# Kernel optimization log

Hardware: AMD Instinct MI355X
Metric: run time of the kernel (lower is better)

## Reference

```python
import jax, jax.numpy as jnp
import numpy as np

EPS = 1e-5

def _ln(x, g, b):
    m = jnp.mean(x, axis=-1, keepdims=True)
    v = jnp.var(x, axis=-1, keepdims=True)
    return (x - m) / jnp.sqrt(v + EPS) * g + b

def setup_inputs() -> dict:
    key = jax.random.key(0)
    ks = jax.random.split(key, 16)
    B, T, N, K, d, E = 2, 12, 512, 8, 64, 64
    D = K * d
    s = 0.02
    inp = {
        "x": jax.random.normal(ks[0], (B, T, N, D), jnp.float32),
        "lapmatrix": jax.random.normal(ks[1], (N, N), jnp.float32),
        "node_embeddings": jax.random.normal(ks[2], (N, E), jnp.float32),
        "Wq": jax.random.normal(ks[3], (D, D), jnp.float32) * s,
        "bq": jnp.zeros((D,), jnp.float32),
        "Wk": jax.random.normal(ks[4], (D, D), jnp.float32) * s,
        "bk": jnp.zeros((D,), jnp.float32),
        "Wv": jax.random.normal(ks[5], (D, D), jnp.float32) * s,
        "bv": jnp.zeros((D,), jnp.float32),
        "Wo": jax.random.normal(ks[6], (D, D), jnp.float32) * s,
        "bo": jnp.zeros((D,), jnp.float32),
        "W1": jax.random.normal(ks[7], (4 * D, D), jnp.float32) * s,
        "b1": jnp.zeros((4 * D,), jnp.float32),
        "W2": jax.random.normal(ks[8], (D, 4 * D), jnp.float32) * s,
        "b2": jnp.zeros((D,), jnp.float32),
        "g1": jnp.ones((D,), jnp.float32),
        "be1": jnp.zeros((D,), jnp.float32),
        "g2": jnp.ones((D,), jnp.float32),
        "be2": jnp.zeros((D,), jnp.float32),
        "alpha": jnp.float32(1.0),
        "beta": jnp.float32(1.0),
        "k": 3,
    }
    return inp

def reference(x, lapmatrix, node_embeddings, Wq, bq, Wk, bk, Wv, bv, Wo, bo,
              W1, b1, W2, b2, g1, be1, g2, be2, alpha, beta, k):
    B, T, N, D = x.shape
    K, d = 8, D // 8
    x_raw = x
    xn = _ln(x, g1, be1)
    q = (xn @ Wq.T + bq).reshape(B, T, N, K, d)
    kk = (xn @ Wk.T + bk).reshape(B, T, N, K, d)
    v = (xn @ Wv.T + bv).reshape(B, T, N, K, d)
    # raw attention logits: [B,T,K,N,N]
    raw = jnp.einsum('btnkd,btmkd->btknm', q, kk) / jnp.sqrt(jnp.float32(d))
    # graph biases, all [N,N], broadcast over B,T,K
    supports = jax.nn.softmax(jax.nn.relu(node_embeddings @ node_embeddings.T), axis=1)
    adj = (lapmatrix != 0).astype(x.dtype)
    mask = jnp.where(adj == 0, jnp.float32(-1e9), jnp.float32(0.0))
    logits = raw + alpha * supports + beta * lapmatrix + mask
    attn = jax.nn.softmax(logits, axis=-1)  # dropout = identity in eval
    out = jnp.einsum('btknm,btmkd->btnkd', attn, v).reshape(B, T, N, D)
    x1 = x_raw + (out @ Wo.T + bo)
    h = _ln(x1, g2, be2)
    ffn = jax.nn.relu(h @ W1.T + b1) @ W2.T + b2
    return x1 + ffn
```

## Files before the change

### kernel.cpp

```cpp
#include <hip/hip_runtime.h>

typedef unsigned short u16;
typedef unsigned int   u32;
typedef __attribute__((ext_vector_type(8))) short bf16x8;
typedef __attribute__((ext_vector_type(4))) float f32x4;

#define DEV static __device__ __forceinline__

DEV float b2f(u16 u){ return __uint_as_float(((u32)u)<<16); }
DEV u16 f2b(float f){
  u32 u = __float_as_uint(f);
  u32 r = (u + 0x7FFFu + ((u>>16)&1u)) >> 16;
  return (u16)r;
}

union V8 { uint4 v; u16 s[8]; };

DEV bool is_f32(const void* dt){ return *(const u32*)dt == 0x3F800000u; }

DEV uint4 ld8_ext_bf(const void* p, size_t i, bool f32){
  if(f32){
    const float* q = (const float*)p + i;
    float4 a = *(const float4*)q, b = *(const float4*)(q+4);
    V8 r;
    r.s[0]=f2b(a.x); r.s[1]=f2b(a.y); r.s[2]=f2b(a.z); r.s[3]=f2b(a.w);
    r.s[4]=f2b(b.x); r.s[5]=f2b(b.y); r.s[6]=f2b(b.z); r.s[7]=f2b(b.w);
    return r.v;
  }
  return *(const uint4*)((const u16*)p + i);
}
DEV void ld8_ext_f(const void* p, size_t i, bool f32, float* o){
  if(f32){
    const float* q = (const float*)p + i;
    float4 a = *(const float4*)q, b = *(const float4*)(q+4);
    o[0]=a.x;o[1]=a.y;o[2]=a.z;o[3]=a.w;o[4]=b.x;o[5]=b.y;o[6]=b.z;o[7]=b.w;
  }else{
    V8 u; u.v = *(const uint4*)((const u16*)p + i);
    #pragma unroll
    for(int k=0;k<8;k++) o[k]=b2f(u.s[k]);
  }
}
DEV float ld1_ext(const void* p, size_t i, bool f32){
  return f32 ? ((const float*)p)[i] : b2f(((const u16*)p)[i]);
}
DEV float load_scalar(const void* p, bool f32){
  return f32 ? *(const float*)p : b2f(*(const u16*)p);
}

DEV void gl_lds16(const u16* g, u16* l){
  __builtin_amdgcn_global_load_lds((const __attribute__((address_space(1))) void*)g,
                                   (__attribute__((address_space(3))) void*)l, 16, 0, 0);
}

__global__ __launch_bounds__(256) void sentinel_kernel(u16* out, long n, const void* dt){
  long ne = is_f32(dt) ? 2*n : n;
  long i = (long)blockIdx.x*256 + threadIdx.x;
  if(i < ne) out[i] = 0x4442;
}

__global__ __launch_bounds__(256) void convert_w_kernel(
    const void* Wq, const void* Wk, const void* Wv, const void* Wo,
    const void* W1, const void* W2, u16* __restrict__ wbf, const void* dt)
{
  const bool f32 = is_f32(dt);
  size_t i = ((size_t)blockIdx.x*256 + threadIdx.x)*8;
  const void* src; size_t base;
  if(i < 262144){ src=Wq; base=0; }
  else if(i < 524288){ src=Wk; base=262144; }
  else if(i < 786432){ src=Wv; base=524288; }
  else if(i < 1048576){ src=Wo; base=786432; }
  else if(i < 2097152){ src=W1; base=1048576; }
  else { src=W2; base=2097152; }
  *(uint4*)(wbf + i) = ld8_ext_bf(src, i-base, f32);
}

__global__ __launch_bounds__(256) void convert_b_kernel(
    const void* bq, const void* bk, const void* bv, const void* bo,
    const void* b1, const void* b2, float* __restrict__ bfp, const void* dt)
{
  const bool f32 = is_f32(dt);
  int j = blockIdx.x*256 + threadIdx.x;
  if(j >= 4608) return;
  const void* src; int off;
  if(j < 512){ src=bq; off=0; }
  else if(j < 1024){ src=bk; off=512; }
  else if(j < 1536){ src=bv; off=1024; }
  else if(j < 2048){ src=bo; off=1536; }
  else if(j < 4096){ src=b1; off=2048; }
  else { src=b2; off=4096; }
  bfp[j] = ld1_ext(src, j-off, f32);
}

__global__ __launch_bounds__(256) void bias_kernel(
    const void* __restrict__ E, const void* __restrict__ lap,
    const void* __restrict__ alpha_p, const void* __restrict__ beta_p,
    float* __restrict__ bm, const void* dt)
{
  __shared__ u16 Et[64*520];
  __shared__ float red[8];
  const bool f32 = is_f32(dt);
  const int t = threadIdx.x, n = blockIdx.x;
  for(int i=0;i<16;i++){
    int c = t + i*256;
    int m = c >> 3, j0 = (c & 7) * 8;
    V8 u; u.v = ld8_ext_bf(E, (size_t)m*64 + j0, f32);
    #pragma unroll
    for(int jj=0;jj<8;jj++) Et[(j0+jj)*520 + m] = u.s[jj];
  }
  __syncthreads();
  const float alpha = load_scalar(alpha_p, f32);
  const float beta  = load_scalar(beta_p, f32);
  float sc0=0.f, sc1=0.f;
  const int m0 = t, m1 = t+256;
  for(int kk=0;kk<64;kk++){
    float en = b2f(Et[kk*520+n]);
    sc0 += en * b2f(Et[kk*520+m0]);
    sc1 += en * b2f(Et[kk*520+m1]);
  }
  sc0 = fmaxf(sc0, 0.f); sc1 = fmaxf(sc1, 0.f);
  float mx = fmaxf(sc0, sc1);
  for(int o=1;o<64;o<<=1) mx = fmaxf(mx, __shfl_xor(mx,o,64));
  const int wave = t>>6;
  if((t&63)==0) red[wave]=mx;
  __syncthreads();
  mx = fmaxf(fmaxf(red[0],red[1]), fmaxf(red[2],red[3]));
  float e0 = __expf(sc0-mx), e1 = __expf(sc1-mx);
  float sm = e0+e1;
  for(int o=1;o<64;o<<=1) sm += __shfl_xor(sm,o,64);
  if((t&63)==0) red[4+wave]=sm;
  __syncthreads();
  sm = red[4]+red[5]+red[6]+red[7];
  const float inv = 1.f/sm;
  float lv0 = ld1_ext(lap, (size_t)n*512+m0, f32);
  bm[n*512+m0] = alpha*e0*inv + beta*lv0 + (lv0==0.f ? -1e9f : 0.f);
  float lv1 = ld1_ext(lap, (size_t)n*512+m1, f32);
  bm[n*512+m1] = alpha*e1*inv + beta*lv1 + (lv1==0.f ? -1e9f : 0.f);
}

template<int EXTIN>
__global__ __launch_bounds__(64) void ln_kernel(const void* __restrict__ xin,
    const void* __restrict__ g, const void* __restrict__ b, u16* __restrict__ out,
    const void* dt)
{
  const bool f32 = is_f32(dt);
  const int row = blockIdx.x, lane = threadIdx.x;
  float v[8];
  if(EXTIN){
    ld8_ext_f(xin, (size_t)row*512 + lane*8, f32, v);
  }else{
    V8 u; u.v = *(const uint4*)((const u16*)xin + (size_t)row*512 + lane*8);
    #pragma unroll
    for(int i=0;i<8;i++) v[i]=b2f(u.s[i]);
  }
  float s=0.f, ss=0.f;
  #pragma unroll
  for(int i=0;i<8;i++){ s+=v[i]; ss+=v[i]*v[i]; }
  #pragma unroll
  for(int o=1;o<64;o<<=1){ s+=__shfl_xor(s,o,64); ss+=__shfl_xor(ss,o,64); }
  const float mean = s*(1.0f/512.0f);
  const float var  = ss*(1.0f/512.0f) - mean*mean;
  const float rstd = rsqrtf(var + 1e-5f);
  float gv[8], bv[8];
  ld8_ext_f(g, (size_t)lane*8, f32, gv);
  ld8_ext_f(b, (size_t)lane*8, f32, bv);
  V8 o8;
  #pragma unroll
  for(int i=0;i<8;i++) o8.s[i]=f2b((v[i]-mean)*rstd*gv[i]+bv[i]);
  *(uint4*)(out+(size_t)row*512+lane*8)=o8.v;
}

template<int RELU, int RES, int RESEXT, int OUTEXT>
__global__ __launch_bounds__(256) void gemm_nt(
    const u16* __restrict__ A, const u16* __restrict__ B,
    const float* __restrict__ bias, const void* __restrict__ resid,
    void* __restrict__ Cout, int N, int K, const void* dt)
{
  __shared__ u16 As[128*64];
  __shared__ u16 Bs[128*64];
  const bool f32 = is_f32(dt);
  const int t = threadIdx.x;
  const int wave = t>>6, lane = t&63;
  const int n0 = blockIdx.y*128, m0 = blockIdx.x*128;
  const int wr = wave>>1, wc = wave&1;

  f32x4 acc[4][4];
  #pragma unroll
  for(int i=0;i<4;i++)
    #pragma unroll
    for(int j=0;j<4;j++){ acc[i][j][0]=0.f; acc[i][j][1]=0.f; acc[i][j][2]=0.f; acc[i][j][3]=0.f; }

  const int lrow8 = lane>>3, lg = lane&7;
  const int gsw = (lg ^ lrow8)*8;
  const u16* Ag = A + (size_t)(m0+lrow8)*K + gsw;
  const u16* Bg = B + (size_t)(n0+lrow8)*K + gsw;
  const int fr = lane&15, qd = lane>>4, frk = (fr&7);

  for(int k0=0; k0<K; k0+=64){
    __syncthreads();
    #pragma unroll
    for(int i=0;i<4;i++){
      int c = wave*4+i;
      gl_lds16(Ag + (size_t)(c*8)*K + k0, &As[c*512]);
      gl_lds16(Bg + (size_t)(c*8)*K + k0, &Bs[c*512]);
    }
    __syncthreads();
    #pragma unroll
    for(int s=0;s<2;s++){
      const int slot = ((s*4+qd) ^ frk)*8;
      bf16x8 af[4], bfr[4];
      #pragma unroll
      for(int i=0;i<4;i++) af[i] = *(const bf16x8*)&As[(wr*64+i*16+fr)*64 + slot];
      #pragma unroll
      for(int j=0;j<4;j++) bfr[j] = *(const bf16x8*)&Bs[(wc*64+j*16+fr)*64 + slot];
      #pragma unroll
      for(int i=0;i<4;i++)
        #pragma unroll
        for(int j=0;j<4;j++)
          acc[i][j] = __builtin_amdgcn_mfma_f32_16x16x32_bf16(af[i], bfr[j], acc[i][j], 0,0,0);
    }
  }

  const int col16 = lane&15, rbase = (lane>>4)*4;
  #pragma unroll
  for(int i=0;i<4;i++){
    #pragma unroll
    for(int j=0;j<4;j++){
      const int gc = n0 + wc*64 + j*16 + col16;
      const float bv = bias[gc];
      #pragma unroll
      for(int r=0;r<4;r++){
        const int gr = m0 + wr*64 + i*16 + rbase + r;
        float val = acc[i][j][r] + bv;
        if(RELU) val = fmaxf(val, 0.f);
        if(RES){
          if(RESEXT) val += ld1_ext(resid, (size_t)gr*N+gc, f32);
          else       val += b2f(((const u16*)resid)[(size_t)gr*N+gc]);
        }
        if(OUTEXT && f32) ((float*)Cout)[(size_t)gr*N+gc] = val;
        else              ((u16*)Cout)[(size_t)gr*N+gc] = f2b(val);
      }
    }
  }
}

template<int RELU, int RES, int RESEXT, int OUTEXT>
__global__ __launch_bounds__(256) void gemm_nt64(
    const u16* __restrict__ A, const u16* __restrict__ B,
    const float* __restrict__ bias, const void* __restrict__ resid,
    void* __restrict__ Cout, int N, int K, const void* dt)
{
  __shared__ u16 As[128*64];
  __shared__ u16 Bs[64*64];
  const bool f32 = is_f32(dt);
  const int t = threadIdx.x;
  const int wave = t>>6, lane = t&63;
  const int n0 = blockIdx.y*64, m0 = blockIdx.x*128;
  const int wr = wave>>1, wc = wave&1;

  f32x4 acc[4][2];
  #pragma unroll
  for(int i=0;i<4;i++)
    #pragma unroll
    for(int j=0;j<2;j++){ acc[i][j][0]=0.f; acc[i][j][1]=0.f; acc[i][j][2]=0.f; acc[i][j][3]=0.f; }

  const int lrow8 = lane>>3, lg = lane&7;
  const int gsw = (lg ^ lrow8)*8;
  const u16* Ag = A + (size_t)(m0+lrow8)*K + gsw;
  const u16* Bg = B + (size_t)(n0+lrow8)*K + gsw;
  const int fr = lane&15, qd = lane>>4, frk = (fr&7);

  for(int k0=0; k0<K; k0+=64){
    __syncthreads();
    #pragma unroll
    for(int i=0;i<4;i++){
      int c = wave*4+i;
      gl_lds16(Ag + (size_t)(c*8)*K + k0, &As[c*512]);
    }
    #pragma unroll
    for(int i=0;i<2;i++){
      int c = wave*2+i;
      gl_lds16(Bg + (size_t)(c*8)*K + k0, &Bs[c*512]);
    }
    __syncthreads();
    #pragma unroll
    for(int s=0;s<2;s++){
      const int slot = ((s*4+qd) ^ frk)*8;
      bf16x8 af[4], bfr[2];
      #pragma unroll
      for(int i=0;i<4;i++) af[i] = *(const bf16x8*)&As[(wr*64+i*16+fr)*64 + slot];
      #pragma unroll
      for(int j=0;j<2;j++) bfr[j] = *(const bf16x8*)&Bs[(wc*32+j*16+fr)*64 + slot];
      #pragma unroll
      for(int i=0;i<4;i++)
        #pragma unroll
        for(int j=0;j<2;j++)
          acc[i][j] = __builtin_amdgcn_mfma_f32_16x16x32_bf16(af[i], bfr[j], acc[i][j], 0,0,0);
    }
  }

  const int col16 = lane&15, rbase = (lane>>4)*4;
  #pragma unroll
  for(int i=0;i<4;i++){
    #pragma unroll
    for(int j=0;j<2;j++){
      const int gc = n0 + wc*32 + j*16 + col16;
      const float bv = bias[gc];
      #pragma unroll
      for(int r=0;r<4;r++){
        const int gr = m0 + wr*64 + i*16 + rbase + r;
        float val = acc[i][j][r] + bv;
        if(RELU) val = fmaxf(val, 0.f);
        if(RES){
          if(RESEXT) val += ld1_ext(resid, (size_t)gr*N+gc, f32);
          else       val += b2f(((const u16*)resid)[(size_t)gr*N+gc]);
        }
        if(OUTEXT && f32) ((float*)Cout)[(size_t)gr*N+gc] = val;
        else              ((u16*)Cout)[(size_t)gr*N+gc] = f2b(val);
      }
    }
  }
}

__global__ __launch_bounds__(256) void attn_kernel(
    const u16* __restrict__ qkv, const float* __restrict__ bm,
    u16* __restrict__ out)
{
  __shared__ u16 Ks[128*72];
  __shared__ u16 Vt[64*136];
  __shared__ u16 P[4][32*72];

  const int QS = 1536;
  const int t = threadIdx.x, wave = t>>6, lane = t&63;
  const int head = blockIdx.y, bt = blockIdx.z;
  const int q0 = blockIdx.x*128 + wave*32;
  const u16* qp = qkv + (size_t)bt*512*QS + head*64;
  const u16* kp = qp + 512;
  const u16* vp = qp + 1024;

  const int l16 = lane&15, qd = lane>>4;

  bf16x8 qf[2][2];
  #pragma unroll
  for(int i=0;i<2;i++)
    #pragma unroll
    for(int kc=0;kc<2;kc++)
      qf[i][kc] = *(const bf16x8*)(qp + (size_t)(q0 + i*16 + l16)*QS + kc*32 + qd*8);

  float mrun[2][4], lrun[2][4];
  #pragma unroll
  for(int i=0;i<2;i++)
    #pragma unroll
    for(int r=0;r<4;r++){ mrun[i][r] = -3e38f; lrun[i][r] = 0.f; }
  f32x4 oacc[2][4];
  #pragma unroll
  for(int i=0;i<2;i++)
    #pragma unroll
    for(int j=0;j<4;j++){ oacc[i][j][0]=0.f; oacc[i][j][1]=0.f; oacc[i][j][2]=0.f; oacc[i][j][3]=0.f; }

  const int srow = t>>1, shalf = (t&1)*32;

  for(int c=0; c<4; c++){
    const u16* kcp = kp + (size_t)(c*128 + srow)*QS + shalf;
    const u16* vcp = vp + (size_t)(c*128 + srow)*QS + shalf;
    uint4 kv[4], vv[4];
    #pragma unroll
    for(int qi=0;qi<4;qi++){ kv[qi] = *(const uint4*)(kcp + qi*8); vv[qi] = *(const uint4*)(vcp + qi*8); }
    __syncthreads();
    #pragma unroll
    for(int qi=0;qi<4;qi++) *(uint4*)&Ks[srow*72 + shalf + qi*8] = kv[qi];
    #pragma unroll
    for(int qi=0;qi<4;qi++){
      V8 u; u.v = vv[qi];
      #pragma unroll
      for(int jj=0;jj<8;jj++) Vt[(shalf + qi*8 + jj)*136 + srow] = u.s[jj];
    }
    __syncthreads();

    f32x4 sacc[2][8];
    #pragma unroll
    for(int tt=0;tt<8;tt++){
      bf16x8 b0 = *(const bf16x8*)&Ks[(tt*16 + l16)*72 +      qd*8];
      bf16x8 b1 = *(const bf16x8*)&Ks[(tt*16 + l16)*72 + 32 + qd*8];
      #pragma unroll
      for(int i=0;i<2;i++){
        f32x4 s; s[0]=0.f; s[1]=0.f; s[2]=0.f; s[3]=0.f;
        s = __builtin_amdgcn_mfma_f32_16x16x32_bf16(qf[i][0], b0, s, 0,0,0);
        s = __builtin_amdgcn_mfma_f32_16x16x32_bf16(qf[i][1], b1, s, 0,0,0);
        sacc[i][tt] = s;
      }
    }

    float cm[2][4];
    #pragma unroll
    for(int i=0;i<2;i++){
      const size_t bb = (size_t)(q0 + i*16 + qd*4)*512 + c*128 + l16;
      #pragma unroll
      for(int r=0;r<4;r++){
        float mxv = -3e38f;
        #pragma unroll
        for(int tt=0;tt<8;tt++){
          float lg2 = sacc[i][tt][r]*0.125f + bm[bb + (size_t)r*512 + tt*16];
          sacc[i][tt][r] = lg2;
          mxv = fmaxf(mxv, lg2);
        }
        cm[i][r] = mxv;
      }
    }
    #pragma unroll
    for(int o=1;o<16;o<<=1)
      #pragma unroll
      for(int i=0;i<2;i++)
        #pragma unroll
        for(int r=0;r<4;r++) cm[i][r] = fmaxf(cm[i][r], __shfl_xor(cm[i][r], o, 64));

    #pragma unroll
    for(int i=0;i<2;i++){
      #pragma unroll
      for(int r=0;r<4;r++){
        float mnew = fmaxf(mrun[i][r], cm[i][r]);
        float al = __expf(mrun[i][r] - mnew);
        mrun[i][r] = mnew;
        float rs = 0.f;
        #pragma unroll
        for(int tt=0;tt<8;tt++){
          float e = __expf(sacc[i][tt][r] - mnew);
          sacc[i][tt][r] = e;
          rs += e;
        }
        lrun[i][r] = lrun[i][r]*al;
        cm[i][r] = rs;
        #pragma unroll
        for(int j=0;j<4;j++) oacc[i][j][r] *= al;
      }
    }
    #pragma unroll
    for(int o=1;o<16;o<<=1)
      #pragma unroll
      for(int i=0;i<2;i++)
        #pragma unroll
        for(int r=0;r<4;r++) cm[i][r] += __shfl_xor(cm[i][r], o, 64);
    #pragma unroll
    for(int i=0;i<2;i++)
      #pragma unroll
      for(int r=0;r<4;r++) lrun[i][r] += cm[i][r];

    u16* Pw = P[wave];
    #pragma unroll
    for(int h=0; h<2; h++){
      #pragma unroll
      for(int i=0;i<2;i++)
        #pragma unroll
        for(int tt=0;tt<4;tt++)
          #pragma unroll
          for(int r=0;r<4;r++)
            Pw[(i*16 + qd*4 + r)*72 + tt*16 + l16] = f2b(sacc[i][h*4+tt][r]);

      #pragma unroll
      for(int ks=0;ks<2;ks++){
        bf16x8 pa[2];
        #pragma unroll
        for(int i=0;i<2;i++)
          pa[i] = *(const bf16x8*)&Pw[(i*16 + l16)*72 + ks*32 + qd*8];
        #pragma unroll
        for(int j=0;j<4;j++){
          bf16x8 bv = *(const bf16x8*)&Vt[(j*16 + l16)*136 + (h*2+ks)*32 + qd*8];
          #pragma unroll
          for(int i=0;i<2;i++)
            oacc[i][j] = __builtin_amdgcn_mfma_f32_16x16x32_bf16(pa[i], bv, oacc[i][j], 0,0,0);
        }
      }
    }
  }

  u16* op = out + (size_t)bt*512*512 + head*64;
  #pragma unroll
  for(int i=0;i<2;i++){
    #pragma unroll
    for(int r=0;r<4;r++){
      const float inv = 1.f / lrun[i][r];
      const size_t rowb = (size_t)(q0 + i*16 + qd*4 + r)*512;
      #pragma unroll
      for(int j=0;j<4;j++)
        op[rowb + j*16 + l16] = f2b(oacc[i][j][r] * inv);
    }
  }
}

extern "C" void kernel_launch(void* const* d_in, const int* in_sizes, int n_in,
                              void* d_out, int out_size, void* d_ws, size_t ws_size,
                              hipStream_t stream) {
  const void* x   = d_in[0];
  const void* lap = d_in[1];
  const void* ne  = d_in[2];
  const void* Wq  = d_in[3];
  const void* bq  = d_in[4];
  const void* Wk  = d_in[5];
  const void* bk  = d_in[6];
  const void* Wv  = d_in[7];
  const void* bv  = d_in[8];
  const void* Wo  = d_in[9];
  const void* bo  = d_in[10];
  const void* W1  = d_in[11];
  const void* b1  = d_in[12];
  const void* W2  = d_in[13];
  const void* b2  = d_in[14];
  const void* g1  = d_in[15];
  const void* be1 = d_in[16];
  const void* g2  = d_in[17];
  const void* be2 = d_in[18];
  const void* alpha = d_in[19];
  const void* beta  = d_in[20];
  const void* dt = g1;

  const int M = 12288;
  const size_t NEED = (size_t)512*512*4 + (size_t)M*512*2*2 + (size_t)M*2048*2
                    + (size_t)3145728*2 + (size_t)4608*4;
  if(ws_size < NEED){
    long n = out_size;
    sentinel_kernel<<<(2*n+255)/256, 256, 0, stream>>>((u16*)d_out, n, dt);
    return;
  }
  char* w = (char*)d_ws;
  float* bias_m = (float*)w;              w += (size_t)512*512*4;
  u16*   slotB  = (u16*)w;                w += (size_t)M*512*2;
  char*  slotC  = w;                      w += (size_t)M*2048*2;
  u16*   x1     = (u16*)w;                w += (size_t)M*512*2;
  u16*   wbf    = (u16*)w;                w += (size_t)3145728*2;
  float* bfp    = (float*)w;
  u16* qkv = (u16*)slotC;
  u16* h1  = (u16*)slotC;
  u16* xn = slotB;
  u16* ao = slotB;
  u16* h  = slotB;

  convert_w_kernel<<<1536, 256, 0, stream>>>(Wq, Wk, Wv, Wo, W1, W2, wbf, dt);
  convert_b_kernel<<<18, 256, 0, stream>>>(bq, bk, bv, bo, b1, b2, bfp, dt);
  bias_kernel<<<512, 256, 0, stream>>>(ne, lap, alpha, beta, bias_m, dt);
  ln_kernel<1><<<M, 64, 0, stream>>>(x, g1, be1, xn, dt);
  gemm_nt<0,0,0,0><<<dim3(96,12), 256, 0, stream>>>(xn, wbf, bfp, nullptr, qkv, 1536, 512, dt);
  attn_kernel<<<dim3(4,8,24), 256, 0, stream>>>(qkv, bias_m, ao);
  gemm_nt64<0,1,1,0><<<dim3(96,8), 256, 0, stream>>>(ao, wbf+786432, bfp+1536, x, x1, 512, 512, dt);
  ln_kernel<0><<<M, 64, 0, stream>>>(x1, g2, be2, h, dt);
  gemm_nt<1,0,0,0><<<dim3(96,16), 256, 0, stream>>>(h, wbf+1048576, bfp+2048, nullptr, h1, 2048, 512, dt);
  gemm_nt64<0,1,0,1><<<dim3(96,8), 256, 0, stream>>>(h1, wbf+2097152, bfp+4096, x1, d_out, 512, 2048, dt);
}
```

Before: 327.8 us.

## Compute transposed S tiles so P stays in registers for PV MFMA

The attention kernel now computes S^T by swapping the MFMA operands (K as A, Q as B) with a permuted K row mapping, so each lane holds scores for a single query row. The softmax then uses a 2-step shuffle reduction, and P is packed to bf16 in registers with v_cvt_pk_bf16 and fed straight to the PV MFMA, removing the per-wave LDS staging buffer and its round trip. Bias loads become float4, the K LDS stride changes to 80, and s_setprio is raised around the MFMA blocks. The risks are correctness of the row permutation, which must line up P with V, and changed bank-conflict behaviour.

```diff
diff --git a/kernel.cpp b/kernel.cpp
--- a/kernel.cpp
+++ b/kernel.cpp
@@ -15,6 +15,12 @@
 }
 
 union V8 { uint4 v; u16 s[8]; };
+
+DEV u32 cvt_pk_bf16(float lo, float hi){
+  u32 r;
+  asm("v_cvt_pk_bf16_f32 %0, %1, %2" : "=v"(r) : "v"(lo), "v"(hi));
+  return r;
+}
 
 DEV bool is_f32(const void* dt){ return *(const u32*)dt == 0x3F800000u; }
 
@@ -325,9 +331,8 @@
     const u16* __restrict__ qkv, const float* __restrict__ bm,
     u16* __restrict__ out)
 {
-  __shared__ u16 Ks[128*72];
+  __shared__ u16 Ks[128*80];
   __shared__ u16 Vt[64*136];
-  __shared__ u16 P[4][32*72];
 
   const int QS = 1536;
   const int t = threadIdx.x, wave = t>>6, lane = t&63;
@@ -346,11 +351,15 @@
     for(int kc=0;kc<2;kc++)
       qf[i][kc] = *(const bf16x8*)(qp + (size_t)(q0 + i*16 + l16)*QS + kc*32 + qd*8);
 
-  float mrun[2][4], lrun[2][4];
-  #pragma unroll
-  for(int i=0;i<2;i++)
-    #pragma unroll
-    for(int r=0;r<4;r++){ mrun[i][r] = -3e38f; lrun[i][r] = 0.f; }
+  const float* bmr0 = bm + (size_t)(q0 + l16)*512;
+  const float* bmr1 = bmr0 + 16*512;
+
+  const int arow = ((l16>>2)<<3) + (l16&3);
+  const u16* KsA = &Ks[arow*80 + qd*8];
+
+  float mrun[2], lrun[2];
+  mrun[0] = -3e38f; mrun[1] = -3e38f;
+  lrun[0] = 0.f;    lrun[1] = 0.f;
   f32x4 oacc[2][4];
   #pragma unroll
   for(int i=0;i<2;i++)
@@ -367,7 +376,7 @@
     for(int qi=0;qi<4;qi++){ kv[qi] = *(const uint4*)(kcp + qi*8); vv[qi] = *(const uint4*)(vcp + qi*8); }
     __syncthreads();
     #pragma unroll
-    for(int qi=0;qi<4;qi++) *(uint4*)&Ks[srow*72 + shalf + qi*8] = kv[qi];
+    for(int qi=0;qi<4;qi++) *(uint4*)&Ks[srow*80 + shalf + qi*8] = kv[qi];
     #pragma unroll
     for(int qi=0;qi<4;qi++){
       V8 u; u.v = vv[qi];
@@ -376,112 +385,93 @@
     }
     __syncthreads();
 
-    f32x4 sacc[2][8];
+    f32x4 p[2][8];
+    __builtin_amdgcn_s_setprio(1);
     #pragma unroll
     for(int tt=0;tt<8;tt++){
-      bf16x8 b0 = *(const bf16x8*)&Ks[(tt*16 + l16)*72 +      qd*8];
-      bf16x8 b1 = *(const bf16x8*)&Ks[(tt*16 + l16)*72 + 32 + qd*8];
+      const int rofs = ((tt&3)*32 + ((tt>>2)<<2))*80;
+      bf16x8 a0 = *(const bf16x8*)(KsA + rofs);
+      bf16x8 a1 = *(const bf16x8*)(KsA + rofs + 32);
       #pragma unroll
       for(int i=0;i<2;i++){
         f32x4 s; s[0]=0.f; s[1]=0.f; s[2]=0.f; s[3]=0.f;
-        s = __builtin_amdgcn_mfma_f32_16x16x32_bf16(qf[i][0], b0, s, 0,0,0);
-        s = __builtin_amdgcn_mfma_f32_16x16x32_bf16(qf[i][1], b1, s, 0,0,0);
-        sacc[i][tt] = s;
-      }
-    }
-
-    float cm[2][4];
+        s = __builtin_amdgcn_mfma_f32_16x16x32_bf16(a0, qf[i][0], s, 0,0,0);
+        s = __builtin_amdgcn_mfma_f32_16x16x32_bf16(a1, qf[i][1], s, 0,0,0);
+        p[i][tt] = s;
+      }
+    }
+    __builtin_amdgcn_s_setprio(0);
+
     #pragma unroll
     for(int i=0;i<2;i++){
-      const size_t bb = (size_t)(q0 + i*16 + qd*4)*512 + c*128 + l16;
+      const float* br = (i ? bmr1 : bmr0) + c*128 + qd*8;
+      float mx = -3e38f;
+      #pragma unroll
+      for(int tt=0;tt<8;tt++){
+        const float4 b4 = *(const float4*)(br + (tt&3)*32 + ((tt>>2)<<2));
+        p[i][tt][0] = p[i][tt][0]*0.125f + b4.x;
+        p[i][tt][1] = p[i][tt][1]*0.125f + b4.y;
+        p[i][tt][2] = p[i][tt][2]*0.125f + b4.z;
+        p[i][tt][3] = p[i][tt][3]*0.125f + b4.w;
+        mx = fmaxf(mx, fmaxf(fmaxf(p[i][tt][0],p[i][tt][1]), fmaxf(p[i][tt][2],p[i][tt][3])));
+      }
+      mx = fmaxf(mx, __shfl_xor(mx, 16, 64));
+      mx = fmaxf(mx, __shfl_xor(mx, 32, 64));
+      const float mnew = fmaxf(mrun[i], mx);
+      const float al = __expf(mrun[i] - mnew);
+      mrun[i] = mnew;
+      float rs = 0.f;
+      #pragma unroll
+      for(int tt=0;tt<8;tt++){
+        p[i][tt][0] = __expf(p[i][tt][0]-mnew);
+        p[i][tt][1] = __expf(p[i][tt][1]-mnew);
+        p[i][tt][2] = __expf(p[i][tt][2]-mnew);
+        p[i][tt][3] = __expf(p[i][tt][3]-mnew);
+        rs += (p[i][tt][0]+p[i][tt][1]) + (p[i][tt][2]+p[i][tt][3]);
+      }
+      rs += __shfl_xor(rs, 16, 64);
+      rs += __shfl_xor(rs, 32, 64);
+      lrun[i] = lrun[i]*al + rs;
       #pragma unroll
       for(int r=0;r<4;r++){
-        float mxv = -3e38f;
+        const float alr = __shfl(al, (qd<<2)+r, 64);
         #pragma unroll
-        for(int tt=0;tt<8;tt++){
-          float lg2 = sacc[i][tt][r]*0.125f + bm[bb + (size_t)r*512 + tt*16];
-          sacc[i][tt][r] = lg2;
-          mxv = fmaxf(mxv, lg2);
-        }
-        cm[i][r] = mxv;
-      }
-    }
-    #pragma unroll
-    for(int o=1;o<16;o<<=1)
-      #pragma unroll
-      for(int i=0;i<2;i++)
-        #pragma unroll
-        for(int r=0;r<4;r++) cm[i][r] = fmaxf(cm[i][r], __shfl_xor(cm[i][r], o, 64));
-
-    #pragma unroll
-    for(int i=0;i<2;i++){
-      #pragma unroll
-      for(int r=0;r<4;r++){
-        float mnew = fmaxf(mrun[i][r], cm[i][r]);
-        float al = __expf(mrun[i][r] - mnew);
-        mrun[i][r] = mnew;
-        float rs = 0.f;
-        #pragma unroll
-        for(int tt=0;tt<8;tt++){
-          float e = __expf(sacc[i][tt][r] - mnew);
-          sacc[i][tt][r] = e;
-          rs += e;
-        }
-        lrun[i][r] = lrun[i][r]*al;
-        cm[i][r] = rs;
-        #pragma unroll
-        for(int j=0;j<4;j++) oacc[i][j][r] *= al;
-      }
-    }
-    #pragma unroll
-    for(int o=1;o<16;o<<=1)
-      #pragma unroll
-      for(int i=0;i<2;i++)
-        #pragma unroll
-        for(int r=0;r<4;r++) cm[i][r] += __shfl_xor(cm[i][r], o, 64);
-    #pragma unroll
-    for(int i=0;i<2;i++)
-      #pragma unroll
-      for(int r=0;r<4;r++) lrun[i][r] += cm[i][r];
-
-    u16* Pw = P[wave];
-    #pragma unroll
-    for(int h=0; h<2; h++){
-      #pragma unroll
-      for(int i=0;i<2;i++)
-        #pragma unroll
-        for(int tt=0;tt<4;tt++)
-          #pragma unroll
-          for(int r=0;r<4;r++)
-            Pw[(i*16 + qd*4 + r)*72 + tt*16 + l16] = f2b(sacc[i][h*4+tt][r]);
-
-      #pragma unroll
-      for(int ks=0;ks<2;ks++){
-        bf16x8 pa[2];
-        #pragma unroll
-        for(int i=0;i<2;i++)
-          pa[i] = *(const bf16x8*)&Pw[(i*16 + l16)*72 + ks*32 + qd*8];
-        #pragma unroll
-        for(int j=0;j<4;j++){
-          bf16x8 bv = *(const bf16x8*)&Vt[(j*16 + l16)*136 + (h*2+ks)*32 + qd*8];
-          #pragma unroll
-          for(int i=0;i<2;i++)
-            oacc[i][j] = __builtin_amdgcn_mfma_f32_16x16x32_bf16(pa[i], bv, oacc[i][j], 0,0,0);
-        }
-      }
-    }
+        for(int j=0;j<4;j++) oacc[i][j][r] *= alr;
+      }
+    }
+
+    __builtin_amdgcn_s_setprio(1);
+    #pragma unroll
+    for(int ks=0;ks<4;ks++){
+      union { bf16x8 v; u32 w[4]; } pa[2];
+      #pragma unroll
+      for(int i=0;i<2;i++){
+        pa[i].w[0] = cvt_pk_bf16(p[i][ks][0],   p[i][ks][1]);
+        pa[i].w[1] = cvt_pk_bf16(p[i][ks][2],   p[i][ks][3]);
+        pa[i].w[2] = cvt_pk_bf16(p[i][ks+4][0], p[i][ks+4][1]);
+        pa[i].w[3] = cvt_pk_bf16(p[i][ks+4][2], p[i][ks+4][3]);
+      }
+      #pragma unroll
+      for(int j=0;j<4;j++){
+        bf16x8 bvf = *(const bf16x8*)&Vt[(j*16 + l16)*136 + ks*32 + qd*8];
+        oacc[0][j] = __builtin_amdgcn_mfma_f32_16x16x32_bf16(pa[0].v, bvf, oacc[0][j], 0,0,0);
+        oacc[1][j] = __builtin_amdgcn_mfma_f32_16x16x32_bf16(pa[1].v, bvf, oacc[1][j], 0,0,0);
+      }
+    }
+    __builtin_amdgcn_s_setprio(0);
   }
 
   u16* op = out + (size_t)bt*512*512 + head*64;
   #pragma unroll
   for(int i=0;i<2;i++){
+    const float inv = 1.f / lrun[i];
     #pragma unroll
     for(int r=0;r<4;r++){
-      const float inv = 1.f / lrun[i][r];
+      const float invr = __shfl(inv, (qd<<2)+r, 64);
       const size_t rowb = (size_t)(q0 + i*16 + qd*4 + r)*512;
       #pragma unroll
       for(int j=0;j<4;j++)
-        op[rowb + j*16 + l16] = f2b(oacc[i][j][r] * inv);
+        op[rowb + j*16 + l16] = f2b(oacc[i][j][r] * invr);
     }
   }
 }
```

After: 333.5 us. No clear change (+1.7%).
